# Optimization experiments

Hardware: AMD Instinct MI355X
Metric: run time of the kernel (lower is better)

The kernel has to match this reference:

```python
import jax, jax.numpy as jnp
import numpy as np

B, S, HID, NH, NS = 2, 1024, 2048, 16, 8
D = HID // NH  # head_dim = 128


def setup_inputs() -> dict:
    key = jax.random.key(0)
    ks = jax.random.split(key, 8)
    inv = 1.0 / np.sqrt(HID)
    return {
        "hidden_states": jax.random.normal(ks[0], (B, S, HID), jnp.float32),
        "Wq": jax.random.normal(ks[1], (HID, HID), jnp.float32) * inv,
        "Wk": jax.random.normal(ks[2], (HID, HID), jnp.float32) * inv,
        "Wv": jax.random.normal(ks[3], (HID, HID), jnp.float32) * inv,
        "Wo": jax.random.normal(ks[4], (HID, HID), jnp.float32) * inv,
        "splat_positions": jax.random.normal(ks[5], (NH, NS, D), jnp.float32) * 0.02,
        "splat_directions": jax.random.normal(ks[6], (NH, NS, D), jnp.float32) * 0.02,
        "splat_log_scales": jnp.full((NH, NS), np.log(0.8), jnp.float32),
        "splat_log_amplitudes": jnp.full((NH, NS), -np.log(float(NS)), jnp.float32),
        "directional_strength": jnp.float32(0.3),
        "gsa_strength": jnp.float32(-6.0),
    }


def _affinities(tokens, positions, directions, scales, dir_strength):
    # tokens [B,NH,S,D]; positions/directions [NH,NS,D]; scales [NH,NS]
    tok_sq = jnp.sum(tokens * tokens, axis=-1)                       # [B,NH,S]
    pos_sq = jnp.sum(positions * positions, axis=-1)                 # [NH,NS]
    tp = jnp.einsum('bhsd,hnd->bhsn', tokens, positions)             # [B,NH,S,NS]
    dist2 = tok_sq[..., None] - 2.0 * tp + pos_sq[None, :, None, :]
    dist2 = jnp.maximum(dist2, 0.0)
    # signed projection of (token - position) onto unit direction
    proj = (jnp.einsum('bhsd,hnd->bhsn', tokens, directions)
            - jnp.sum(positions * directions, axis=-1)[None, :, None, :])
    perp2 = jnp.maximum(dist2 - proj * proj, 0.0)
    inv2s2 = (0.5 / (scales * scales))[None, :, None, :]
    radial = jnp.exp(-dist2 * inv2s2)
    directional = jnp.exp(-perp2 * inv2s2)
    return (1.0 - dir_strength) * radial + dir_strength * directional


def reference(hidden_states, Wq, Wk, Wv, Wo, splat_positions, splat_directions,
              splat_log_scales, splat_log_amplitudes, directional_strength, gsa_strength):
    b, s, hid = hidden_states.shape

    def heads(x):  # [B,S,HID] -> [B,NH,S,D]
        return x.reshape(b, s, NH, D).transpose(0, 2, 1, 3)

    q = heads(hidden_states @ Wq)
    k = heads(hidden_states @ Wk)
    v = heads(hidden_states @ Wv)

    # --- standard (original) attention path ---
    scores = jnp.einsum('bhqd,bhkd->bhqk', q, k) / jnp.sqrt(jnp.float32(D))
    attn = jax.nn.softmax(scores, axis=-1)
    std = jnp.einsum('bhqk,bhkd->bhqd', attn, v)
    std = std.transpose(0, 2, 1, 3).reshape(b, s, hid) @ Wo

    # --- directional GSA path ---
    eps = 1e-12
    positions = splat_positions / (jnp.linalg.norm(splat_positions, axis=-1, keepdims=True) + eps)
    positions = positions * (np.sqrt(D) * 0.3)
    directions = splat_directions / (jnp.linalg.norm(splat_directions, axis=-1, keepdims=True) + eps)
    scales = jnp.clip(jnp.exp(splat_log_scales), 0.3, 1.2)
    amplitudes = jax.nn.softmax(splat_log_amplitudes, axis=-1)
    ds = jax.nn.sigmoid(directional_strength)

    qa = _affinities(q, positions, directions, scales, ds)  # [B,NH,S,NS]
    ka = _affinities(k, positions, directions, scales, ds)  # [B,NH,S,NS]
    w = jnp.einsum('bhqn,hn,bhkn->bhqk', qa, amplitudes, ka)
    w = w / (jnp.sum(w, axis=-1, keepdims=True) + 1e-8)
    dgsa = jnp.einsum('bhqk,bhkd->bhqd', w, v)
    dgsa = dgsa.transpose(0, 2, 1, 3).reshape(b, s, hid) @ Wo

    gsa = jax.nn.sigmoid(gsa_strength)
    blend = jnp.minimum(0.05, gsa * 0.1)
    return (1.0 - blend) * std + blend * dgsa
```

## Files before the change

kernel.cpp:

```cpp
#include <hip/hip_runtime.h>
#include <math.h>

typedef __attribute__((ext_vector_type(8))) short bf16x8;
typedef __attribute__((ext_vector_type(4))) float f32x4;
typedef unsigned short ushort_t;

#define SQRT_D 11.313708498984761f
#define INV_SQRT_D 0.08838834764831845f

__device__ __forceinline__ unsigned short f2b(float f) {
    unsigned u = __float_as_uint(f);
    unsigned r = (u + 0x7fffu + ((u >> 16) & 1u)) >> 16;
    return (unsigned short)r;
}
__device__ __forceinline__ float b2f(unsigned short h) {
    return __uint_as_float(((unsigned)h) << 16);
}

__device__ __forceinline__ void async_copy16(const void* g, void* l) {
    __builtin_amdgcn_global_load_lds((const __attribute__((address_space(1))) void*)g,
                                     (__attribute__((address_space(3))) void*)l, 16, 0, 0);
}

__global__ __launch_bounds__(256) void prep(
    const float* __restrict__ X, const float* __restrict__ W0,
    const float* __restrict__ W1, const float* __restrict__ W2,
    const float* __restrict__ W3, const float* __restrict__ sp,
    const float* __restrict__ sd, const float* __restrict__ ls,
    const float* __restrict__ la, ushort_t* __restrict__ Xbf,
    ushort_t* __restrict__ WT4, float* __restrict__ posn,
    float* __restrict__ dirn, float* __restrict__ pos_sq,
    float* __restrict__ pdv, float* __restrict__ iv2s2,
    float* __restrict__ amp) {
    __shared__ float t[32][33];
    const int z = blockIdx.z;
    if (z < 4) {
        const float* W = (z == 0) ? W0 : (z == 1) ? W1 : (z == 2) ? W2 : W3;
        ushort_t* WT = WT4 + (size_t)z * 4194304;
        int tx = threadIdx.x & 31, ty = threadIdx.x >> 5;
        int bn = blockIdx.x * 32, bk = blockIdx.y * 32;
#pragma unroll
        for (int i = 0; i < 4; ++i)
            t[ty + i * 8][tx] = W[(size_t)(bk + ty + i * 8) * 2048 + bn + tx];
        __syncthreads();
#pragma unroll
        for (int i = 0; i < 4; ++i)
            WT[(size_t)(bn + ty + i * 8) * 2048 + bk + tx] = f2b(t[tx][ty + i * 8]);
        return;
    }
    {
        int bi = blockIdx.y * 64 + blockIdx.x;
        int i = (bi * 256 + threadIdx.x) * 4;
        float4 v = *(const float4*)(X + i);
        ushort4 o;
        o.x = f2b(v.x); o.y = f2b(v.y); o.z = f2b(v.z); o.w = f2b(v.w);
        *(ushort4*)(Xbf + i) = o;
    }
    if (blockIdx.x == 0 && blockIdx.y == 0 && threadIdx.x < 128) {
        int i = threadIdx.x;
        const float* p = sp + (size_t)i * 128;
        const float* d = sd + (size_t)i * 128;
        float np_ = 0.f, nd_ = 0.f;
        for (int k = 0; k < 128; ++k) { np_ += p[k] * p[k]; nd_ += d[k] * d[k]; }
        np_ = sqrtf(np_); nd_ = sqrtf(nd_);
        const float sc = 3.394112549695428f;
        float rp = sc / (np_ + 1e-12f);
        float rd = 1.f / (nd_ + 1e-12f);
        float psq = 0.f, pd_ = 0.f;
        for (int k = 0; k < 128; ++k) {
            float pn = p[k] * rp;
            float dn = d[k] * rd;
            posn[(size_t)i * 128 + k] = pn;
            dirn[(size_t)i * 128 + k] = dn;
            psq += pn * pn;
            pd_ += pn * dn;
        }
        pos_sq[i] = psq;
        pdv[i] = pd_;
        float s = expf(ls[i]);
        s = fminf(fmaxf(s, 0.3f), 1.2f);
        iv2s2[i] = 0.5f / (s * s);
        if ((i & 7) == 0) {
            int h = i >> 3;
            float mx = -INFINITY;
            for (int n = 0; n < 8; ++n) mx = fmaxf(mx, la[h * 8 + n]);
            float e[8]; float ssum = 0.f;
            for (int n = 0; n < 8; ++n) { e[n] = expf(la[h * 8 + n] - mx); ssum += e[n]; }
            for (int n = 0; n < 8; ++n) amp[h * 8 + n] = e[n] / ssum;
        }
    }
}


__global__ __launch_bounds__(256) void gemm_qkv(const ushort_t* __restrict__ A,
                                                const ushort_t* __restrict__ WT4,
                                                ushort_t* __restrict__ Qb,
                                                ushort_t* __restrict__ Kb,
                                                ushort_t* __restrict__ Vb,
                                                ushort_t* __restrict__ Vt) {
    __shared__ ushort_t As[2][128 * 32];
    __shared__ ushort_t Bs[2][128 * 32];
    const int tid = threadIdx.x, lane = tid & 63, wave = tid >> 6;
    const int l15 = lane & 15, quad = lane >> 4;
    const int wm = (wave >> 1) * 64, wn = (wave & 1) * 64;
    const int bm = blockIdx.x * 128;
    const int by = blockIdx.y, which = by >> 4, bn = (by & 15) * 128;
    const ushort_t* BT = WT4 + (size_t)which * 4194304;
    f32x4 acc[4][4] = {};
    const int off0 = tid * 16;
    const int row0 = tid >> 2;
    const int c0 = (tid & 3) ^ ((row0 + (row0 >> 2)) & 3);
    const ushort_t* ga = A + (size_t)(bm + row0) * 2048 + c0 * 8;
    const ushort_t* gb = BT + (size_t)(bn + row0) * 2048 + c0 * 8;
    const int rsw = (l15 + (l15 >> 2)) & 3;
#define STAGEG(buf_, k_)                                                      \
    {                                                                         \
        async_copy16(ga + (k_), (char*)As[buf_] + off0);                      \
        async_copy16(ga + (size_t)64 * 2048 + (k_), (char*)As[buf_] + off0 + 4096); \
        async_copy16(gb + (k_), (char*)Bs[buf_] + off0);                      \
        async_copy16(gb + (size_t)64 * 2048 + (k_), (char*)Bs[buf_] + off0 + 4096); \
    }
    STAGEG(0, 0);
    for (int k0 = 0; k0 < 2048; k0 += 32) {
        __syncthreads();
        if (k0 < 2016) STAGEG(((k0 >> 5) + 1) & 1, k0 + 32);
        const int cb = (k0 >> 5) & 1;
        bf16x8 af[4], bfr[4];
#pragma unroll
        for (int i = 0; i < 4; ++i)
            af[i] = *(const bf16x8*)((const char*)As[cb] + (wm + i * 16 + l15) * 64 + ((quad ^ rsw) << 4));
#pragma unroll
        for (int j = 0; j < 4; ++j)
            bfr[j] = *(const bf16x8*)((const char*)Bs[cb] + (wn + j * 16 + l15) * 64 + ((quad ^ rsw) << 4));
#pragma unroll
        for (int i = 0; i < 4; ++i)
#pragma unroll
            for (int j = 0; j < 4; ++j)
                acc[i][j] = __builtin_amdgcn_mfma_f32_16x16x32_bf16(af[i], bfr[j], acc[i][j], 0, 0, 0);
    }
#undef STAGEG
    ushort_t* Cb = (which == 0) ? Qb : ((which == 1) ? Kb : Vb);
    const bool dot = (which == 2);
    const float oscale = (which == 0) ? INV_SQRT_D : 1.f;
#pragma unroll
    for (int i = 0; i < 4; ++i) {
#pragma unroll
        for (int j = 0; j < 4; ++j) {
            int m0 = bm + wm + i * 16 + quad * 4;
            int n = bn + wn + j * 16 + l15;
            int b = m0 >> 10, s0 = m0 & 1023, h = n >> 7, d = n & 127;
            ushort4 pack;
            unsigned short* pp = (unsigned short*)&pack;
#pragma unroll
            for (int r = 0; r < 4; ++r) {
                unsigned short bv = f2b(acc[i][j][r] * oscale);
                pp[r] = bv;
                Cb[((size_t)((b << 4) | h) * 1024 + (s0 + r)) * 128 + d] = bv;
            }
            if (dot) *(ushort4*)(Vt + ((size_t)((b << 4) | h) * 128 + d) * 1024 + s0) = pack;
        }
    }
}

__global__ __launch_bounds__(256) void gemm_out(const ushort_t* __restrict__ A,
                                                const ushort_t* __restrict__ BT,
                                                float* __restrict__ Cf) {
    __shared__ ushort_t As[2][128 * 32];
    __shared__ ushort_t Bs[2][64 * 32];
    const int tid = threadIdx.x, lane = tid & 63, wave = tid >> 6;
    const int l15 = lane & 15, quad = lane >> 4;
    const int wm = (wave >> 1) * 64, wn = (wave & 1) * 32;
    const int bm = blockIdx.x * 128, bn = blockIdx.y * 64;
    f32x4 acc[4][2] = {};
    const int off0 = tid * 16;
    const int row0 = tid >> 2;
    const int c0 = (tid & 3) ^ ((row0 + (row0 >> 2)) & 3);
    const ushort_t* ga = A + (size_t)(bm + row0) * 2048 + c0 * 8;
    const ushort_t* gb = BT + (size_t)(bn + row0) * 2048 + c0 * 8;
    const int rsw = (l15 + (l15 >> 2)) & 3;
#define STAGEO(buf_, k_)                                                      \
    {                                                                         \
        async_copy16(ga + (k_), (char*)As[buf_] + off0);                      \
        async_copy16(ga + (size_t)64 * 2048 + (k_), (char*)As[buf_] + off0 + 4096); \
        async_copy16(gb + (k_), (char*)Bs[buf_] + off0);                      \
    }
    STAGEO(0, 0);
    for (int k0 = 0; k0 < 2048; k0 += 32) {
        __syncthreads();
        if (k0 < 2016) STAGEO(((k0 >> 5) + 1) & 1, k0 + 32);
        const int cb = (k0 >> 5) & 1;
        bf16x8 af[4], bfr[2];
#pragma unroll
        for (int i = 0; i < 4; ++i)
            af[i] = *(const bf16x8*)((const char*)As[cb] + (wm + i * 16 + l15) * 64 + ((quad ^ rsw) << 4));
#pragma unroll
        for (int j = 0; j < 2; ++j)
            bfr[j] = *(const bf16x8*)((const char*)Bs[cb] + (wn + j * 16 + l15) * 64 + ((quad ^ rsw) << 4));
#pragma unroll
        for (int i = 0; i < 4; ++i)
#pragma unroll
            for (int j = 0; j < 2; ++j)
                acc[i][j] = __builtin_amdgcn_mfma_f32_16x16x32_bf16(af[i], bfr[j], acc[i][j], 0, 0, 0);
    }
#undef STAGEO
#pragma unroll
    for (int i = 0; i < 4; ++i)
#pragma unroll
        for (int j = 0; j < 2; ++j)
#pragma unroll
            for (int r = 0; r < 4; ++r) {
                int m = bm + wm + i * 16 + quad * 4 + r;
                int n = bn + wn + j * 16 + l15;
                Cf[(size_t)m * 2048 + n] = acc[i][j][r];
            }
}

__global__ __launch_bounds__(256) void affinity_k(
    const ushort_t* __restrict__ K,
    const float* __restrict__ posn, const float* __restrict__ dirn,
    const float* __restrict__ pos_sq, const float* __restrict__ pdv,
    const float* __restrict__ iv2s2, const float* __restrict__ ds_in,
    float* __restrict__ ka) {
    int gid = blockIdx.x * 256 + threadIdx.x;
    int n = gid & 7;
    int t = gid >> 3;
    const ushort_t* T = K + (size_t)t * 128;
    int h = (t >> 10) & 15;
    const float* P = posn + (size_t)(h * 8 + n) * 128;
    const float* Dr = dirn + (size_t)(h * 8 + n) * 128;
    float tsq = 0.f, tp = 0.f, td = 0.f;
#pragma unroll
    for (int d = 0; d < 128; d += 8) {
        uint4 raw = *(const uint4*)(T + d);
        float tv[8];
        tv[0] = __uint_as_float(raw.x << 16); tv[1] = __uint_as_float(raw.x & 0xffff0000u);
        tv[2] = __uint_as_float(raw.y << 16); tv[3] = __uint_as_float(raw.y & 0xffff0000u);
        tv[4] = __uint_as_float(raw.z << 16); tv[5] = __uint_as_float(raw.z & 0xffff0000u);
        tv[6] = __uint_as_float(raw.w << 16); tv[7] = __uint_as_float(raw.w & 0xffff0000u);
        float4 p0 = *(const float4*)(P + d), p1 = *(const float4*)(P + d + 4);
        float4 d0 = *(const float4*)(Dr + d), d1 = *(const float4*)(Dr + d + 4);
        tsq += tv[0]*tv[0]+tv[1]*tv[1]+tv[2]*tv[2]+tv[3]*tv[3]+tv[4]*tv[4]+tv[5]*tv[5]+tv[6]*tv[6]+tv[7]*tv[7];
        tp  += tv[0]*p0.x+tv[1]*p0.y+tv[2]*p0.z+tv[3]*p0.w+tv[4]*p1.x+tv[5]*p1.y+tv[6]*p1.z+tv[7]*p1.w;
        td  += tv[0]*d0.x+tv[1]*d0.y+tv[2]*d0.z+tv[3]*d0.w+tv[4]*d1.x+tv[5]*d1.y+tv[6]*d1.z+tv[7]*d1.w;
    }
    float dist2 = fmaxf(tsq - 2.f * tp + pos_sq[h * 8 + n], 0.f);
    float proj = td - pdv[h * 8 + n];
    float perp2 = fmaxf(dist2 - proj * proj, 0.f);
    float iv = iv2s2[h * 8 + n];
    float dsv = 1.f / (1.f + __expf(-ds_in[0]));
    float aff = (1.f - dsv) * __expf(-dist2 * iv) + dsv * __expf(-perp2 * iv);
    ka[(size_t)t * 8 + n] = aff;
}

__global__ __launch_bounds__(128) void kv_s1_part(const float* __restrict__ ka,
                                                  const ushort_t* __restrict__ V,
                                                  float* __restrict__ KVp,
                                                  float* __restrict__ S1p) {
    int bh = blockIdx.x, sc = blockIdx.y;
    int d = threadIdx.x;
    const float* kaB = ka + ((size_t)bh * 1024 + sc * 128) * 8;
    const ushort_t* VB = V + ((size_t)bh * 1024 + sc * 128) * 128;
    float acc[8] = {};
#pragma unroll 4
    for (int s = 0; s < 128; ++s) {
        float vd = b2f(VB[(size_t)s * 128 + d]);
        float4 k0 = *(const float4*)(kaB + (size_t)s * 8);
        float4 k1 = *(const float4*)(kaB + (size_t)s * 8 + 4);
        acc[0] += k0.x * vd; acc[1] += k0.y * vd; acc[2] += k0.z * vd; acc[3] += k0.w * vd;
        acc[4] += k1.x * vd; acc[5] += k1.y * vd; acc[6] += k1.z * vd; acc[7] += k1.w * vd;
    }
#pragma unroll
    for (int n = 0; n < 8; ++n) KVp[(((size_t)bh * 8 + n) * 8 + sc) * 128 + d] = acc[n];
    __shared__ float s1p[128];
    {
        int n = d >> 4, chunk = d & 15;
        float p = 0.f;
        for (int s = chunk * 8; s < chunk * 8 + 8; ++s) p += kaB[(size_t)s * 8 + n];
        s1p[d] = p;
    }
    __syncthreads();
    if (d < 8) {
        float t = 0.f;
        for (int c = 0; c < 16; ++c) t += s1p[(d << 4) + c];
        S1p[((size_t)bh * 8 + d) * 8 + sc] = t;
    }
}

__global__ __launch_bounds__(256) void flash_blend(
    const ushort_t* __restrict__ Qg, const ushort_t* __restrict__ Kg,
    const ushort_t* __restrict__ Vtg,
    const float* __restrict__ posn, const float* __restrict__ dirn,
    const float* __restrict__ pos_sq, const float* __restrict__ pdv,
    const float* __restrict__ iv2s2, const float* __restrict__ ds_in,
    const float* __restrict__ amp,
    const float* __restrict__ S1p, const float* __restrict__ KVp,
    const float* __restrict__ gstr, ushort_t* __restrict__ blended) {
    __shared__ ushort_t Ks[2][64 * 128];
    __shared__ ushort_t Vt[2][128 * 64];
    __shared__ ushort_t Ps[4][16 * 72];
    __shared__ float KVs[8 * 128];
    __shared__ float S1s[8];
    __shared__ float qas[4][16][8];
    const int tid = threadIdx.x, lane = tid & 63, wave = tid >> 6;
    const int l15 = lane & 15, quad = lane >> 4;
    const int bh = blockIdx.y, qt = blockIdx.x;
    const int h = bh & 15;

    const ushort_t* Qrow = Qg + ((size_t)(bh * 1024 + qt * 64 + wave * 16 + l15)) * 128 + quad * 8;
    bf16x8 aq[4];
#pragma unroll
    for (int k4 = 0; k4 < 4; ++k4) aq[k4] = *(const bf16x8*)(Qrow + k4 * 32);

    {
        float tsq = 0.f, tp[8] = {}, td[8] = {};
#pragma unroll
        for (int k4 = 0; k4 < 4; ++k4) {
#pragma unroll
            for (int j = 0; j < 8; ++j) {
                float qv = b2f((unsigned short)aq[k4][j]) * SQRT_D;
                int d = k4 * 32 + quad * 8 + j;
                tsq += qv * qv;
#pragma unroll
                for (int n = 0; n < 8; ++n) {
                    tp[n] += qv * posn[(size_t)(h * 8 + n) * 128 + d];
                    td[n] += qv * dirn[(size_t)(h * 8 + n) * 128 + d];
                }
            }
        }
        tsq += __shfl_xor(tsq, 16); tsq += __shfl_xor(tsq, 32);
        float dsv = 1.f / (1.f + __expf(-ds_in[0]));
#pragma unroll
        for (int n = 0; n < 8; ++n) {
            float a = tp[n]; a += __shfl_xor(a, 16); a += __shfl_xor(a, 32);
            float bb = td[n]; bb += __shfl_xor(bb, 16); bb += __shfl_xor(bb, 32);
            float dist2 = fmaxf(tsq - 2.f * a + pos_sq[h * 8 + n], 0.f);
            float proj = bb - pdv[h * 8 + n];
            float perp2 = fmaxf(dist2 - proj * proj, 0.f);
            float iv = iv2s2[h * 8 + n];
            float aff = (1.f - dsv) * __expf(-dist2 * iv) + dsv * __expf(-perp2 * iv);
            if (quad == 0) qas[wave][l15][n] = aff;
        }
    }

    {
        int n = tid >> 5, d = (tid & 31) * 4;
        f32x4 kv = {};
#pragma unroll
        for (int sc = 0; sc < 8; ++sc)
            kv += *(const f32x4*)(KVp + (((size_t)bh * 8 + n) * 8 + sc) * 128 + d);
        *(f32x4*)(KVs + tid * 4) = kv;
    }
    if (tid < 8) {
        float s = 0.f;
#pragma unroll
        for (int sc = 0; sc < 8; ++sc) s += S1p[((size_t)bh * 8 + tid) * 8 + sc];
        S1s[tid] = s;
    }

    const ushort_t* Kbase = Kg + (size_t)bh * 131072;
    const ushort_t* Vbase = Vtg + (size_t)bh * 131072;

#define STAGE(buf, kt_)                                                               \
    {                                                                                 \
        _Pragma("unroll") for (int i_ = 0; i_ < 4; ++i_) {                            \
            int off_ = tid * 16 + i_ * 4096;                                          \
            int kr_ = off_ >> 8, kp_ = (off_ >> 4) & 15;                              \
            async_copy16(Kbase + (size_t)(kt_)*8192 + kr_ * 128 + ((kp_ ^ (kr_ & 15)) << 3), \
                         (char*)(&Ks[buf][0]) + off_);                                \
            int vd_ = off_ >> 7, vp_ = (off_ >> 4) & 7;                               \
            async_copy16(Vbase + (size_t)vd_ * 1024 + (kt_)*64 + ((vp_ ^ (vd_ & 7)) << 3), \
                         (char*)(&Vt[buf][0]) + off_);                                \
        }                                                                             \
    }

    STAGE(0, 0);

    f32x4 o[8] = {};
    float l_i[4] = {};
    ushort_t* Pw = &Ps[wave][0];

    for (int kt = 0; kt < 16; ++kt) {
        __syncthreads();
        if (kt < 15) STAGE((kt + 1) & 1, kt + 1);
        const int cb = kt & 1;
        f32x4 sc[4] = {};
#pragma unroll
        for (int k4 = 0; k4 < 4; ++k4) {
#pragma unroll
            for (int t = 0; t < 4; ++t) {
                bf16x8 bk = *(const bf16x8*)((const char*)&Ks[cb][0] +
                                             ((t * 16 + l15) << 8) + (((k4 * 4 + quad) ^ l15) << 4));
                sc[t] = __builtin_amdgcn_mfma_f32_16x16x32_bf16(aq[k4], bk, sc[t], 0, 0, 0);
            }
        }
#pragma unroll
        for (int t = 0; t < 4; ++t) {
#pragma unroll
            for (int r = 0; r < 4; ++r) {
                float p = __expf(sc[t][r]);
                l_i[r] += p;
                Pw[(quad * 4 + r) * 72 + t * 16 + l15] = f2b(p);
            }
        }
        bf16x8 ap0 = *(const bf16x8*)((const char*)Pw + (l15 * 72 + quad * 8) * 2);
        bf16x8 ap1 = *(const bf16x8*)((const char*)Pw + (l15 * 72 + 32 + quad * 8) * 2);
#pragma unroll
        for (int j = 0; j < 8; ++j) {
            bf16x8 bv0 = *(const bf16x8*)((const char*)&Vt[cb][0] +
                                          ((j * 16 + l15) << 7) + (((quad) ^ (l15 & 7)) << 4));
            bf16x8 bv1 = *(const bf16x8*)((const char*)&Vt[cb][0] +
                                          ((j * 16 + l15) << 7) + (((4 + quad) ^ (l15 & 7)) << 4));
            o[j] = __builtin_amdgcn_mfma_f32_16x16x32_bf16(ap0, bv0, o[j], 0, 0, 0);
            o[j] = __builtin_amdgcn_mfma_f32_16x16x32_bf16(ap1, bv1, o[j], 0, 0, 0);
        }
    }
#undef STAGE
#pragma unroll
    for (int r = 0; r < 4; ++r) {
        float l = l_i[r];
        l += __shfl_xor(l, 1);
        l += __shfl_xor(l, 2);
        l += __shfl_xor(l, 4);
        l += __shfl_xor(l, 8);
        l_i[r] = l;
    }
    float gsa = 1.f / (1.f + __expf(-gstr[0]));
    float blend = fminf(0.05f, gsa * 0.1f);
    int b = bh >> 4;
#pragma unroll
    for (int r = 0; r < 4; ++r) {
        int q = qt * 64 + wave * 16 + quad * 4 + r;
        float qam[8], Z = 0.f;
#pragma unroll
        for (int n = 0; n < 8; ++n) {
            qam[n] = qas[wave][quad * 4 + r][n] * amp[h * 8 + n];
            Z += qam[n] * S1s[n];
        }
        float invZ = 1.f / (Z + 1e-8f);
        float invl = 1.f / l_i[r];
        ushort_t* outp = blended + ((size_t)(b * 1024 + q)) * 2048 + h * 128;
#pragma unroll
        for (int j = 0; j < 8; ++j) {
            int d = j * 16 + l15;
            float dg = 0.f;
#pragma unroll
            for (int n = 0; n < 8; ++n) dg += qam[n] * KVs[n * 128 + d];
            float v = (1.f - blend) * (o[j][r] * invl) + blend * (dg * invZ);
            outp[d] = f2b(v);
        }
    }
}

extern "C" void kernel_launch(void* const* d_in, const int* in_sizes, int n_in,
                              void* d_out, int out_size, void* d_ws, size_t ws_size,
                              hipStream_t stream) {
    const float* X = (const float*)d_in[0];
    const float* Wq = (const float*)d_in[1];
    const float* Wk = (const float*)d_in[2];
    const float* Wv = (const float*)d_in[3];
    const float* Wo = (const float*)d_in[4];
    const float* sp = (const float*)d_in[5];
    const float* sd = (const float*)d_in[6];
    const float* ls = (const float*)d_in[7];
    const float* la = (const float*)d_in[8];
    const float* dstr = (const float*)d_in[9];
    const float* gstr = (const float*)d_in[10];

    char* base = (char*)d_ws;
    ushort_t* WT4 = (ushort_t*)base;      base += 33554432;
    ushort_t* Xbf = (ushort_t*)base;      base += 8388608;
    ushort_t* blended = Xbf;
    ushort_t* Qbf = (ushort_t*)base;      base += 8388608;
    ushort_t* Kbf = (ushort_t*)base;      base += 8388608;
    ushort_t* Vbf = (ushort_t*)base;      base += 8388608;
    ushort_t* Vtb = (ushort_t*)base;      base += 8388608;
    float* kaw = (float*)base;            base += 1048576;
    float* posn = (float*)base;           base += 65536;
    float* dirn = (float*)base;           base += 65536;
    float* pos_sq = (float*)base;         base += 512;
    float* pdv = (float*)base;            base += 512;
    float* iv2s2 = (float*)base;          base += 512;
    float* ampw = (float*)base;           base += 512;
    float* S1p = (float*)base;            base += 8192;
    float* KVp = (float*)base;            base += 1048576;

    prep<<<dim3(64, 64, 5), 256, 0, stream>>>(X, Wq, Wk, Wv, Wo, sp, sd, ls, la,
                                              Xbf, WT4, posn, dirn, pos_sq, pdv, iv2s2, ampw);
    gemm_qkv<<<dim3(16, 48), 256, 0, stream>>>(Xbf, WT4, Qbf, Kbf, Vbf, Vtb);
    affinity_k<<<1024, 256, 0, stream>>>(Kbf, posn, dirn, pos_sq, pdv, iv2s2, dstr, kaw);
    kv_s1_part<<<dim3(32, 8), 128, 0, stream>>>(kaw, Vbf, KVp, S1p);
    flash_blend<<<dim3(16, 32), 256, 0, stream>>>(Qbf, Kbf, Vtb, posn, dirn, pos_sq, pdv,
                                                  iv2s2, dstr, ampw, S1p, KVp, gstr, blended);
    gemm_out<<<dim3(16, 32), 256, 0, stream>>>(blended, WT4 + 12582912, (float*)d_out);
}
```

Measured before the change: 374.1 us.

## Fuse K affinity into kv_s1_part and move Q affinity out of flash kernel

K-side splat affinities are now computed inside kv_s1_part and kept in shared memory, so the separate affinity kernel and its global round trip for K go away. The Q-side affinity computation moves out of flash_blend into a standalone kernel that writes qa to global memory, and flash_blend reads it back in the epilogue. This shortens the flash kernel's prologue and lowers its register pressure, at the cost of one extra global read of qa and a serial per-thread 128-dim dot-product loop in the small kv_s1_part grid.

```diff
diff --git a/kernel.cpp b/kernel.cpp
--- a/kernel.cpp
+++ b/kernel.cpp
@@ -215,16 +215,16 @@
             }
 }
 
-__global__ __launch_bounds__(256) void affinity_k(
-    const ushort_t* __restrict__ K,
+__global__ __launch_bounds__(256) void affinity_q(
+    const ushort_t* __restrict__ Q,
     const float* __restrict__ posn, const float* __restrict__ dirn,
     const float* __restrict__ pos_sq, const float* __restrict__ pdv,
     const float* __restrict__ iv2s2, const float* __restrict__ ds_in,
-    float* __restrict__ ka) {
+    float* __restrict__ qa) {
     int gid = blockIdx.x * 256 + threadIdx.x;
     int n = gid & 7;
     int t = gid >> 3;
-    const ushort_t* T = K + (size_t)t * 128;
+    const ushort_t* T = Q + (size_t)t * 128;
     int h = (t >> 10) & 15;
     const float* P = posn + (size_t)(h * 8 + n) * 128;
     const float* Dr = dirn + (size_t)(h * 8 + n) * 128;
@@ -243,31 +243,62 @@
         tp  += tv[0]*p0.x+tv[1]*p0.y+tv[2]*p0.z+tv[3]*p0.w+tv[4]*p1.x+tv[5]*p1.y+tv[6]*p1.z+tv[7]*p1.w;
         td  += tv[0]*d0.x+tv[1]*d0.y+tv[2]*d0.z+tv[3]*d0.w+tv[4]*d1.x+tv[5]*d1.y+tv[6]*d1.z+tv[7]*d1.w;
     }
+    const float fs = SQRT_D;
+    tsq *= fs * fs; tp *= fs; td *= fs;
     float dist2 = fmaxf(tsq - 2.f * tp + pos_sq[h * 8 + n], 0.f);
     float proj = td - pdv[h * 8 + n];
     float perp2 = fmaxf(dist2 - proj * proj, 0.f);
     float iv = iv2s2[h * 8 + n];
     float dsv = 1.f / (1.f + __expf(-ds_in[0]));
     float aff = (1.f - dsv) * __expf(-dist2 * iv) + dsv * __expf(-perp2 * iv);
-    ka[(size_t)t * 8 + n] = aff;
-}
-
-__global__ __launch_bounds__(128) void kv_s1_part(const float* __restrict__ ka,
-                                                  const ushort_t* __restrict__ V,
-                                                  float* __restrict__ KVp,
-                                                  float* __restrict__ S1p) {
+    qa[(size_t)t * 8 + n] = aff;
+}
+
+__global__ __launch_bounds__(128) void kv_s1_part(
+    const ushort_t* __restrict__ K, const ushort_t* __restrict__ V,
+    const float* __restrict__ posn, const float* __restrict__ dirn,
+    const float* __restrict__ pos_sq, const float* __restrict__ pdv,
+    const float* __restrict__ iv2s2, const float* __restrict__ ds_in,
+    float* __restrict__ KVp, float* __restrict__ S1p) {
+    __shared__ float kas[128][8];
     int bh = blockIdx.x, sc = blockIdx.y;
-    int d = threadIdx.x;
-    const float* kaB = ka + ((size_t)bh * 1024 + sc * 128) * 8;
+    int tid = threadIdx.x;
+    int h = bh & 15;
+    {
+        const ushort_t* T = K + ((size_t)bh * 1024 + sc * 128 + tid) * 128;
+        float tsq = 0.f, tp[8] = {}, td[8] = {};
+        for (int d = 0; d < 128; d += 4) {
+            uint2 raw = *(const uint2*)(T + d);
+            float t0 = __uint_as_float(raw.x << 16), t1 = __uint_as_float(raw.x & 0xffff0000u);
+            float t2 = __uint_as_float(raw.y << 16), t3 = __uint_as_float(raw.y & 0xffff0000u);
+            tsq += t0 * t0 + t1 * t1 + t2 * t2 + t3 * t3;
+#pragma unroll
+            for (int n = 0; n < 8; ++n) {
+                const float* P = posn + (size_t)(h * 8 + n) * 128 + d;
+                const float* Dr = dirn + (size_t)(h * 8 + n) * 128 + d;
+                tp[n] += t0 * P[0] + t1 * P[1] + t2 * P[2] + t3 * P[3];
+                td[n] += t0 * Dr[0] + t1 * Dr[1] + t2 * Dr[2] + t3 * Dr[3];
+            }
+        }
+        float dsv = 1.f / (1.f + __expf(-ds_in[0]));
+#pragma unroll
+        for (int n = 0; n < 8; ++n) {
+            float dist2 = fmaxf(tsq - 2.f * tp[n] + pos_sq[h * 8 + n], 0.f);
+            float proj = td[n] - pdv[h * 8 + n];
+            float perp2 = fmaxf(dist2 - proj * proj, 0.f);
+            float iv = iv2s2[h * 8 + n];
+            kas[tid][n] = (1.f - dsv) * __expf(-dist2 * iv) + dsv * __expf(-perp2 * iv);
+        }
+    }
+    __syncthreads();
+    int d = tid;
     const ushort_t* VB = V + ((size_t)bh * 1024 + sc * 128) * 128;
     float acc[8] = {};
 #pragma unroll 4
     for (int s = 0; s < 128; ++s) {
         float vd = b2f(VB[(size_t)s * 128 + d]);
-        float4 k0 = *(const float4*)(kaB + (size_t)s * 8);
-        float4 k1 = *(const float4*)(kaB + (size_t)s * 8 + 4);
-        acc[0] += k0.x * vd; acc[1] += k0.y * vd; acc[2] += k0.z * vd; acc[3] += k0.w * vd;
-        acc[4] += k1.x * vd; acc[5] += k1.y * vd; acc[6] += k1.z * vd; acc[7] += k1.w * vd;
+#pragma unroll
+        for (int n = 0; n < 8; ++n) acc[n] += kas[s][n] * vd;
     }
 #pragma unroll
     for (int n = 0; n < 8; ++n) KVp[(((size_t)bh * 8 + n) * 8 + sc) * 128 + d] = acc[n];
@@ -275,7 +306,7 @@
     {
         int n = d >> 4, chunk = d & 15;
         float p = 0.f;
-        for (int s = chunk * 8; s < chunk * 8 + 8; ++s) p += kaB[(size_t)s * 8 + n];
+        for (int s = chunk * 8; s < chunk * 8 + 8; ++s) p += kas[s][n];
         s1p[d] = p;
     }
     __syncthreads();
@@ -289,10 +320,7 @@
 __global__ __launch_bounds__(256) void flash_blend(
     const ushort_t* __restrict__ Qg, const ushort_t* __restrict__ Kg,
     const ushort_t* __restrict__ Vtg,
-    const float* __restrict__ posn, const float* __restrict__ dirn,
-    const float* __restrict__ pos_sq, const float* __restrict__ pdv,
-    const float* __restrict__ iv2s2, const float* __restrict__ ds_in,
-    const float* __restrict__ amp,
+    const float* __restrict__ qa, const float* __restrict__ amp,
     const float* __restrict__ S1p, const float* __restrict__ KVp,
     const float* __restrict__ gstr, ushort_t* __restrict__ blended) {
     __shared__ ushort_t Ks[2][64 * 128];
@@ -300,47 +328,14 @@
     __shared__ ushort_t Ps[4][16 * 72];
     __shared__ float KVs[8 * 128];
     __shared__ float S1s[8];
-    __shared__ float qas[4][16][8];
     const int tid = threadIdx.x, lane = tid & 63, wave = tid >> 6;
     const int l15 = lane & 15, quad = lane >> 4;
     const int bh = blockIdx.y, qt = blockIdx.x;
-    const int h = bh & 15;
 
     const ushort_t* Qrow = Qg + ((size_t)(bh * 1024 + qt * 64 + wave * 16 + l15)) * 128 + quad * 8;
     bf16x8 aq[4];
 #pragma unroll
     for (int k4 = 0; k4 < 4; ++k4) aq[k4] = *(const bf16x8*)(Qrow + k4 * 32);
-
-    {
-        float tsq = 0.f, tp[8] = {}, td[8] = {};
-#pragma unroll
-        for (int k4 = 0; k4 < 4; ++k4) {
-#pragma unroll
-            for (int j = 0; j < 8; ++j) {
-                float qv = b2f((unsigned short)aq[k4][j]) * SQRT_D;
-                int d = k4 * 32 + quad * 8 + j;
-                tsq += qv * qv;
-#pragma unroll
-                for (int n = 0; n < 8; ++n) {
-                    tp[n] += qv * posn[(size_t)(h * 8 + n) * 128 + d];
-                    td[n] += qv * dirn[(size_t)(h * 8 + n) * 128 + d];
-                }
-            }
-        }
-        tsq += __shfl_xor(tsq, 16); tsq += __shfl_xor(tsq, 32);
-        float dsv = 1.f / (1.f + __expf(-ds_in[0]));
-#pragma unroll
-        for (int n = 0; n < 8; ++n) {
-            float a = tp[n]; a += __shfl_xor(a, 16); a += __shfl_xor(a, 32);
-            float bb = td[n]; bb += __shfl_xor(bb, 16); bb += __shfl_xor(bb, 32);
-            float dist2 = fmaxf(tsq - 2.f * a + pos_sq[h * 8 + n], 0.f);
-            float proj = bb - pdv[h * 8 + n];
-            float perp2 = fmaxf(dist2 - proj * proj, 0.f);
-            float iv = iv2s2[h * 8 + n];
-            float aff = (1.f - dsv) * __expf(-dist2 * iv) + dsv * __expf(-perp2 * iv);
-            if (quad == 0) qas[wave][l15][n] = aff;
-        }
-    }
 
     {
         int n = tid >> 5, d = (tid & 31) * 4;
@@ -426,14 +421,15 @@
     }
     float gsa = 1.f / (1.f + __expf(-gstr[0]));
     float blend = fminf(0.05f, gsa * 0.1f);
-    int b = bh >> 4;
+    int b = bh >> 4, h = bh & 15;
 #pragma unroll
     for (int r = 0; r < 4; ++r) {
         int q = qt * 64 + wave * 16 + quad * 4 + r;
+        const float* qaRow = qa + ((size_t)bh * 1024 + q) * 8;
         float qam[8], Z = 0.f;
 #pragma unroll
         for (int n = 0; n < 8; ++n) {
-            qam[n] = qas[wave][quad * 4 + r][n] * amp[h * 8 + n];
+            qam[n] = qaRow[n] * amp[h * 8 + n];
             Z += qam[n] * S1s[n];
         }
         float invZ = 1.f / (Z + 1e-8f);
@@ -474,7 +470,7 @@
     ushort_t* Kbf = (ushort_t*)base;      base += 8388608;
     ushort_t* Vbf = (ushort_t*)base;      base += 8388608;
     ushort_t* Vtb = (ushort_t*)base;      base += 8388608;
-    float* kaw = (float*)base;            base += 1048576;
+    float* qaw = (float*)base;            base += 1048576;
     float* posn = (float*)base;           base += 65536;
     float* dirn = (float*)base;           base += 65536;
     float* pos_sq = (float*)base;         base += 512;
@@ -487,9 +483,10 @@
     prep<<<dim3(64, 64, 5), 256, 0, stream>>>(X, Wq, Wk, Wv, Wo, sp, sd, ls, la,
                                               Xbf, WT4, posn, dirn, pos_sq, pdv, iv2s2, ampw);
     gemm_qkv<<<dim3(16, 48), 256, 0, stream>>>(Xbf, WT4, Qbf, Kbf, Vbf, Vtb);
-    affinity_k<<<1024, 256, 0, stream>>>(Kbf, posn, dirn, pos_sq, pdv, iv2s2, dstr, kaw);
-    kv_s1_part<<<dim3(32, 8), 128, 0, stream>>>(kaw, Vbf, KVp, S1p);
-    flash_blend<<<dim3(16, 32), 256, 0, stream>>>(Qbf, Kbf, Vtb, posn, dirn, pos_sq, pdv,
-                                                  iv2s2, dstr, ampw, S1p, KVp, gstr, blended);
+    affinity_q<<<1024, 256, 0, stream>>>(Qbf, posn, dirn, pos_sq, pdv, iv2s2, dstr, qaw);
+    kv_s1_part<<<dim3(32, 8), 128, 0, stream>>>(Kbf, Vbf, posn, dirn, pos_sq, pdv, iv2s2,
+                                                dstr, KVp, S1p);
+    flash_blend<<<dim3(16, 32), 256, 0, stream>>>(Qbf, Kbf, Vtb, qaw, ampw, S1p, KVp,
+                                                  gstr, blended);
     gemm_out<<<dim3(16, 32), 256, 0, stream>>>(blended, WT4 + 12582912, (float*)d_out);
 }
```

Result: faster. 345.9 us (-7.5%).
